# Kernel optimization log

Measured on AMD Instinct MI355X. Metric: run time of the kernel, lower is better.

Reference implementation:

```python
import jax, jax.numpy as jnp
import numpy as np

B, D = 4096, 1024
N_CLASSES = 100
INF = jnp.float32(3.4e38)


def setup_inputs() -> dict:
    key = jax.random.key(0)
    k1, k2 = jax.random.split(key)
    x = jax.random.normal(k1, (B, 1, D), dtype=jnp.float32)
    labels = jax.random.randint(k2, (B,), 0, N_CLASSES)
    return {"x": x, "labels": labels}


def _awareness_scan(xs, labels_f, R_init):
    # xs: [B, D] float32, labels_f: [B] float32
    b, d = xs.shape
    slots = jnp.arange(b)

    def step(state, inp):
        refs, ref_labels, n_refs, count, min_d, max_d, R = state
        xi, li = inp
        mask = slots < n_refs  # active reference slots
        # distances from candidate to current reference set (torch.cdist, p=2)
        d_all = jnp.sqrt(jnp.sum((refs - xi[None, :]) ** 2, axis=-1))  # [B]
        d_all = jax.lax.stop_gradient(d_all)
        d_act = jnp.where(mask, d_all, INF)
        min_act = jnp.min(d_act)
        is_first = count == 1
        # new reference iff ALL active distances exceed R (i.e. min > R)
        insert = is_first | (min_act > R)
        refs2 = jnp.where(insert, refs.at[n_refs].set(xi), refs)
        ref_labels2 = jnp.where(insert, ref_labels.at[n_refs].set(li), ref_labels)
        n_refs2 = n_refs + insert.astype(n_refs.dtype)
        # dynamic ray update (skipped on the very first sample, as in torch)
        max_act = jnp.max(jnp.where(mask, d_all, -INF))
        min_d2 = jnp.where(is_first, min_d, jnp.minimum(min_d, min_act))
        max_d2 = jnp.where(is_first, max_d, jnp.maximum(max_d, max_act))
        R2 = jnp.where(is_first, R, (min_d2 + max_d2) / 3)
        # prediction: nearest reference AFTER potential insertion
        mask2 = slots < n_refs2
        d2 = jnp.sqrt(jnp.sum((refs2 - xi[None, :]) ** 2, axis=-1))
        d2 = jax.lax.stop_gradient(d2)
        idx = jnp.argmin(jnp.where(mask2, d2, INF))
        pred = ref_labels2[idx]
        new_state = (refs2, ref_labels2, n_refs2, count + 1, min_d2, max_d2, R2)
        return new_state, pred

    init = (
        jnp.zeros((b, d), jnp.float32),   # reference instances buffer
        jnp.zeros((b,), jnp.float32),     # reference labels buffer
        jnp.int32(0),                     # n_refs
        jnp.int32(1),                     # count (starts at 1, as in torch)
        INF,                              # min_dist
        jnp.float32(0.0),                 # max_dist
        jnp.float32(R_init),              # R
    )
    _, preds = jax.lax.scan(step, init, (xs, labels_f))
    return preds  # [B] float32


def reference(x, labels):
    # x: [B, 1, D]; labels: [B] int. update_ref_insts=True, set_labels=labels.
    xs = x.reshape(x.shape[0], x.shape[2])
    labels_f = labels.astype(jnp.float32)
    return _awareness_scan(xs, labels_f, 1.0)
```

## Files before the change

kernel.cpp:

```cpp
#include <hip/hip_runtime.h>
#include <stdint.h>

#define B_N   4096
#define D_DIM 1024
#define INF_F 3.4e38f

typedef float floatx4 __attribute__((ext_vector_type(4)));

#define XQ_OFF 131072

__global__ __launch_bounds__(256)
void k_prep(const float* __restrict__ x, unsigned char* __restrict__ xq,
            float* __restrict__ norms,
            unsigned long long* __restrict__ minpack,
            unsigned int* __restrict__ maxbits) {
    const int row = blockIdx.x;
    const int t   = threadIdx.x;
    float4 v = ((const float4*)x)[row * 256 + t];
    int p = __builtin_amdgcn_cvt_pk_fp8_f32(v.x, v.y, 0, false);
    p     = __builtin_amdgcn_cvt_pk_fp8_f32(v.z, v.w, p, true);
    ((int*)xq)[row * 256 + t] = p;
    float s = v.x * v.x + v.y * v.y + v.z * v.z + v.w * v.w;
    #pragma unroll
    for (int off = 32; off; off >>= 1) s += __shfl_down(s, off);
    __shared__ float ws4[4];
    if ((t & 63) == 0) ws4[t >> 6] = s;
    __syncthreads();
    if (t == 0) {
        norms[row]   = ws4[0] + ws4[1] + ws4[2] + ws4[3];
        minpack[row] = 0xFFFFFFFFFFFFFFFFull;
        maxbits[row] = 0u;
    }
}

#define GLDS(g, l)                                                              \
    __builtin_amdgcn_global_load_lds(                                           \
        (__attribute__((address_space(1))) void*)(void*)(g),                    \
        (__attribute__((address_space(3))) void*)(void*)(l), 16, 0, 0)

__global__ __launch_bounds__(256, 2)
void k_pass1_fp8(const unsigned char* __restrict__ xq,
                 const float* __restrict__ norms,
                 unsigned long long* __restrict__ minpack,
                 unsigned int* __restrict__ maxbits) {
    int bid = blockIdx.x;
    int ti  = (int)((sqrtf(8.f * bid + 1.f) - 1.f) * 0.5f);
    while ((ti + 1) * (ti + 2) / 2 <= bid) ti++;
    while (ti * (ti + 1) / 2 > bid) ti--;
    int tj  = bid - ti * (ti + 1) / 2;

    __shared__ unsigned char As[2][16384];
    __shared__ unsigned char Bs[2][16384];
    __shared__ unsigned long long redMin[128][2];
    __shared__ float redMax[128][2];

    const int t    = threadIdx.x;
    const int w    = t >> 6, lane = t & 63;
    const int wm   = w >> 1, wn = w & 1;
    const int q4   = lane >> 4, c15 = lane & 15;
    const int i0   = ti * 128, j0 = tj * 128;

    const int sr = lane >> 3;
    const int sc = (lane & 7) ^ (sr & 7);

    const unsigned char* gA[4]; const unsigned char* gB[4];
    int eoff[4];
    #pragma unroll
    for (int q = 0; q < 4; q++) {
        int e   = w * 4 + q;
        int row = e * 8 + sr;
        gA[q] = xq + (size_t)(i0 + row) * D_DIM + sc * 16;
        gB[q] = xq + (size_t)(j0 + row) * D_DIM + sc * 16;
        eoff[q] = e * 1024;
    }

    const int r7 = c15 & 7;
    int oib[4];
    #pragma unroll
    for (int kk = 0; kk < 4; kk++) {
        int sl  = kk * 2 + (q4 >> 1);
        oib[kk] = (((sl ^ r7) << 4) | ((q4 & 1) << 3));
    }
    int rbA[4], rbB[4];
    #pragma unroll
    for (int st = 0; st < 4; st++) {
        rbA[st] = (wm * 64 + st * 16 + c15) * 128;
        rbB[st] = (wn * 64 + st * 16 + c15) * 128;
    }

    floatx4 acc[4][4];
    #pragma unroll
    for (int m = 0; m < 4; m++)
        #pragma unroll
        for (int n = 0; n < 4; n++)
            acc[m][n] = (floatx4){0.f, 0.f, 0.f, 0.f};

    #pragma unroll
    for (int q = 0; q < 4; q++) {
        GLDS(gA[q], As[0] + eoff[q]);
        GLDS(gB[q], Bs[0] + eoff[q]);
        gA[q] += 128; gB[q] += 128;
    }

    #pragma unroll 2
    for (int it = 0; it < 8; it++) {
        const int p = it & 1;
        if (it < 7) {
            #pragma unroll
            for (int q = 0; q < 4; q++) {
                GLDS(gA[q], As[p ^ 1] + eoff[q]);
                GLDS(gB[q], Bs[p ^ 1] + eoff[q]);
                gA[q] += 128; gB[q] += 128;
            }
            asm volatile("s_waitcnt vmcnt(8)" ::: "memory");
        } else {
            asm volatile("s_waitcnt vmcnt(0)" ::: "memory");
        }
        __builtin_amdgcn_s_barrier();

        const unsigned char* Ap = As[p];
        const unsigned char* Bp = Bs[p];
        #pragma unroll
        for (int kk = 0; kk < 4; kk++) {
            long long af[4], bfr[4];
            #pragma unroll
            for (int st = 0; st < 4; st++) {
                af[st]  = *(const long long*)(Ap + rbA[st] + oib[kk]);
                bfr[st] = *(const long long*)(Bp + rbB[st] + oib[kk]);
            }
            #pragma unroll
            for (int m = 0; m < 4; m++)
                #pragma unroll
                for (int n = 0; n < 4; n++)
                    acc[m][n] = __builtin_amdgcn_mfma_f32_16x16x32_fp8_fp8(
                        af[m], bfr[n], acc[m][n], 0, 0, 0);
        }
        asm volatile("s_waitcnt lgkmcnt(0)" ::: "memory");
        __builtin_amdgcn_s_barrier();
    }

    float nj[4];
    #pragma unroll
    for (int st = 0; st < 4; st++) nj[st] = norms[j0 + wn * 64 + st * 16 + c15];

    #pragma unroll
    for (int st_m = 0; st_m < 4; st_m++) {
        #pragma unroll
        for (int r = 0; r < 4; r++) {
            int i_loc = wm * 64 + st_m * 16 + q4 * 4 + r;
            int gi    = i0 + i_loc;
            float ni  = norms[gi];
            unsigned long long mp = 0xFFFFFFFFFFFFFFFFull;
            float mx = -INF_F;
            #pragma unroll
            for (int st_n = 0; st_n < 4; st_n++) {
                int gj = j0 + wn * 64 + st_n * 16 + c15;
                if (gj < gi) {
                    float dot = acc[st_m][st_n][r];
                    float d2  = fmaxf(ni + nj[st_n] - 2.f * dot, 0.f);
                    unsigned long long p =
                        ((unsigned long long)__float_as_uint(d2) << 32) | (unsigned)gj;
                    if (p < mp) mp = p;
                    mx = fmaxf(mx, d2);
                }
            }
            #pragma unroll
            for (int off = 1; off < 16; off <<= 1) {
                unsigned long long op = __shfl_xor(mp, off, 64);
                if (op < mp) mp = op;
                float om = __shfl_xor(mx, off, 64);
                mx = fmaxf(mx, om);
            }
            if (c15 == 0) { redMin[i_loc][wn] = mp; redMax[i_loc][wn] = mx; }
        }
    }
    __syncthreads();
    if (t < 128) {
        unsigned long long mp = redMin[t][0];
        if (redMin[t][1] < mp) mp = redMin[t][1];
        float mx = fmaxf(redMax[t][0], redMax[t][1]);
        if (mp != 0xFFFFFFFFFFFFFFFFull) {
            atomicMin(&minpack[i0 + t], mp);
            atomicMax(&maxbits[i0 + t], __float_as_uint(mx));
        }
    }
}

__global__ __launch_bounds__(1024)
void k_tail(const unsigned long long* __restrict__ minpack,
            const unsigned int* __restrict__ maxbits,
            const float* __restrict__ x, const float* __restrict__ norms,
            const int* __restrict__ labels, int* __restrict__ ref_idx,
            float* __restrict__ out) {
    const int t    = threadIdx.x;
    const int lane = t & 63, wid = t >> 6;
    float m[4], M[4];
    #pragma unroll
    for (int q = 0; q < 4; q++) {
        int i = t * 4 + q;
        unsigned long long p = minpack[i];
        float dmin = (p == 0xFFFFFFFFFFFFFFFFull)
                       ? INF_F : sqrtf(__uint_as_float((unsigned)(p >> 32)));
        m[q] = (i == 0) ? INF_F : dmin;
        M[q] = (i == 0) ? -INF_F : sqrtf(__uint_as_float(maxbits[i]));
    }
    float pmin[4], pmax[4];
    pmin[0] = m[0]; pmax[0] = M[0];
    #pragma unroll
    for (int q = 1; q < 4; q++) {
        pmin[q] = fminf(pmin[q - 1], m[q]);
        pmax[q] = fmaxf(pmax[q - 1], M[q]);
    }
    float wmin = pmin[3], wmax = pmax[3];
    #pragma unroll
    for (int off = 1; off < 64; off <<= 1) {
        float a = __shfl_up(wmin, off, 64);
        float b = __shfl_up(wmax, off, 64);
        if (lane >= off) { wmin = fminf(wmin, a); wmax = fmaxf(wmax, b); }
    }
    __shared__ float swmin[16], swmax[16];
    if (lane == 63) { swmin[wid] = wmin; swmax[wid] = wmax; }
    __syncthreads();
    float exwMin = INF_F, exwMax = -INF_F;
    for (int k = 0; k < wid; k++) {
        exwMin = fminf(exwMin, swmin[k]);
        exwMax = fmaxf(exwMax, swmax[k]);
    }
    float upMin = __shfl_up(wmin, 1, 64);
    float upMax = __shfl_up(wmax, 1, 64);
    float exMin = fminf(exwMin, (lane > 0) ? upMin : INF_F);
    float exMax = fmaxf(exwMax, (lane > 0) ? upMax : -INF_F);

    int viol = B_N;
    #pragma unroll
    for (int q = 0; q < 4; q++) {
        int i = t * 4 + q;
        if (i >= 1) {
            float pm = (q == 0) ? exMin : fminf(exMin, pmin[q - 1]);
            float pM = (q == 0) ? exMax : fmaxf(exMax, pmax[q - 1]);
            float R  = (i == 1) ? 1.0f : (pm + pM) / 3.0f;
            if (!(m[q] > R) && i < viol) viol = i;
        }
    }
    int vw = viol;
    #pragma unroll
    for (int off = 32; off; off >>= 1) vw = min(vw, __shfl_down(vw, off, 64));
    __shared__ int svw[16];
    if (lane == 0) svw[wid] = vw;
    __syncthreads();
    int s_star = B_N;
    for (int k = 0; k < 16; k++) s_star = min(s_star, svw[k]);

    for (int i = t; i < s_star; i += 1024) out[i] = (float)labels[i];

    __shared__ float s_state[3];
    __shared__ int s_n;
    if (s_star < B_N && t == (s_star >> 2)) {
        int q = s_star & 3;
        float pm = (q == 0) ? exMin : fminf(exMin, pmin[q - 1]);
        float pM = (q == 0) ? exMax : fmaxf(exMax, pmax[q - 1]);
        float md = fminf(pm, m[q]);
        float Md = fmaxf(pM, M[q]);
        s_state[0] = md; s_state[1] = Md; s_state[2] = (md + Md) / 3.0f;
        s_n = s_star;
        unsigned long long p = minpack[s_star];
        int j = (int)(unsigned)(p & 0xFFFFFFFFu);
        out[s_star] = (float)labels[j];
    }
    if (s_star >= B_N) return;

    for (int s = t; s < s_star; s += 1024) ref_idx[s] = s;
    __syncthreads();

    __shared__ unsigned long long redp[1024];
    __shared__ float redm[1024];
    for (int i = s_star + 1; i < B_N; i++) {
        int n = s_n;
        const float* xi = x + (size_t)i * D_DIM;
        float ni = norms[i];
        unsigned long long mp = 0xFFFFFFFFFFFFFFFFull;
        float mx = -INF_F;
        for (int slot = t; slot < n; slot += 1024) {
            int j = ref_idx[slot];
            const float* xj = x + (size_t)j * D_DIM;
            float dot = 0.f;
            for (int k = 0; k < D_DIM; k++) dot = fmaf(xi[k], xj[k], dot);
            float d = sqrtf(fmaxf(ni + norms[j] - 2.f * dot, 0.f));
            unsigned long long p =
                ((unsigned long long)__float_as_uint(d) << 32) | (unsigned)slot;
            if (p < mp) mp = p;
            mx = fmaxf(mx, d);
        }
        redp[t] = mp; redm[t] = mx;
        __syncthreads();
        for (int off = 512; off; off >>= 1) {
            if (t < off) {
                if (redp[t + off] < redp[t]) redp[t] = redp[t + off];
                redm[t] = fmaxf(redm[t], redm[t + off]);
            }
            __syncthreads();
        }
        if (t == 0) {
            unsigned long long p = redp[0];
            float min_act = __uint_as_float((unsigned)(p >> 32));
            int minslot   = (int)(unsigned)(p & 0xFFFFFFFFu);
            float max_act = redm[0];
            bool insert = (min_act > s_state[2]);
            int pred;
            if (insert) {
                ref_idx[n] = i;
                s_n = n + 1;
                pred = (min_act <= 0.0f) ? labels[ref_idx[minslot]] : labels[i];
            } else {
                pred = labels[ref_idx[minslot]];
            }
            float md = fminf(s_state[0], min_act);
            float Md = fmaxf(s_state[1], max_act);
            s_state[0] = md; s_state[1] = Md; s_state[2] = (md + Md) / 3.0f;
            out[i] = (float)pred;
        }
        __syncthreads();
    }
}

extern "C" void kernel_launch(void* const* d_in, const int* in_sizes, int n_in,
                              void* d_out, int out_size, void* d_ws, size_t ws_size,
                              hipStream_t stream) {
    const float* x      = (const float*)d_in[0];
    const int*   labels = (const int*)d_in[1];
    float*       out    = (float*)d_out;
    char* ws = (char*)d_ws;
    unsigned long long* minpack = (unsigned long long*)ws;
    unsigned int*       maxbits = (unsigned int*)(ws + 32768);
    float*              norms   = (float*)(ws + 49152);
    int*                ref_idx = (int*)(ws + 65600);
    unsigned char*      xq      = (unsigned char*)(ws + XQ_OFF);

    k_prep<<<B_N, 256, 0, stream>>>(x, xq, norms, minpack, maxbits);
    const int ntiles  = B_N / 128;
    const int nblocks = ntiles * (ntiles + 1) / 2;
    k_pass1_fp8<<<nblocks, 256, 0, stream>>>(xq, norms, minpack, maxbits);
    k_tail<<<1, 1024, 0, stream>>>(minpack, maxbits, x, norms, labels, ref_idx, out);
}
```

Before: 105.8 us.

## Use 512-thread blocks with single-buffered LDS in fp8 distance pass

The fp8 MFMA Gram kernel now runs 8 waves per block in a 4x2 layout. Each wave computes a 32x64 sub-tile instead of 64x64, which halves the accumulators per thread. The double-buffered LDS prefetch with manual waitcnt is replaced by a single buffer guarded by two __syncthreads per k-step, and launch bounds rise to allow more resident waves. The intent is to hide global-load latency through occupancy rather than software pipelining, at the cost of losing explicit load/compute overlap and adding more barriers.

```diff
diff --git a/kernel.cpp b/kernel.cpp
--- a/kernel.cpp
+++ b/kernel.cpp
@@ -38,7 +38,7 @@
         (__attribute__((address_space(1))) void*)(void*)(g),                    \
         (__attribute__((address_space(3))) void*)(void*)(l), 16, 0, 0)
 
-__global__ __launch_bounds__(256, 2)
+__global__ __launch_bounds__(512, 6)
 void k_pass1_fp8(const unsigned char* __restrict__ xq,
                  const float* __restrict__ norms,
                  unsigned long long* __restrict__ minpack,
@@ -49,8 +49,8 @@
     while (ti * (ti + 1) / 2 > bid) ti--;
     int tj  = bid - ti * (ti + 1) / 2;
 
-    __shared__ unsigned char As[2][16384];
-    __shared__ unsigned char Bs[2][16384];
+    __shared__ unsigned char As[16384];
+    __shared__ unsigned char Bs[16384];
     __shared__ unsigned long long redMin[128][2];
     __shared__ float redMax[128][2];
 
@@ -63,15 +63,16 @@
     const int sr = lane >> 3;
     const int sc = (lane & 7) ^ (sr & 7);
 
-    const unsigned char* gA[4]; const unsigned char* gB[4];
-    int eoff[4];
-    #pragma unroll
-    for (int q = 0; q < 4; q++) {
-        int e   = w * 4 + q;
+    const unsigned char* gA[2]; const unsigned char* gB[2];
+    unsigned char* lA[2]; unsigned char* lB[2];
+    #pragma unroll
+    for (int q = 0; q < 2; q++) {
+        int e   = w * 2 + q;
         int row = e * 8 + sr;
         gA[q] = xq + (size_t)(i0 + row) * D_DIM + sc * 16;
         gB[q] = xq + (size_t)(j0 + row) * D_DIM + sc * 16;
-        eoff[q] = e * 1024;
+        lA[q] = As + e * 1024;
+        lB[q] = Bs + e * 1024;
     }
 
     const int r7 = c15 & 7;
@@ -81,62 +82,44 @@
         int sl  = kk * 2 + (q4 >> 1);
         oib[kk] = (((sl ^ r7) << 4) | ((q4 & 1) << 3));
     }
-    int rbA[4], rbB[4];
-    #pragma unroll
-    for (int st = 0; st < 4; st++) {
-        rbA[st] = (wm * 64 + st * 16 + c15) * 128;
-        rbB[st] = (wn * 64 + st * 16 + c15) * 128;
-    }
-
-    floatx4 acc[4][4];
-    #pragma unroll
-    for (int m = 0; m < 4; m++)
+    int rbA[2], rbB[4];
+    #pragma unroll
+    for (int st = 0; st < 2; st++) rbA[st] = (wm * 32 + st * 16 + c15) * 128;
+    #pragma unroll
+    for (int st = 0; st < 4; st++) rbB[st] = (wn * 64 + st * 16 + c15) * 128;
+
+    floatx4 acc[2][4];
+    #pragma unroll
+    for (int m = 0; m < 2; m++)
         #pragma unroll
         for (int n = 0; n < 4; n++)
             acc[m][n] = (floatx4){0.f, 0.f, 0.f, 0.f};
 
-    #pragma unroll
-    for (int q = 0; q < 4; q++) {
-        GLDS(gA[q], As[0] + eoff[q]);
-        GLDS(gB[q], Bs[0] + eoff[q]);
-        gA[q] += 128; gB[q] += 128;
-    }
-
-    #pragma unroll 2
     for (int it = 0; it < 8; it++) {
-        const int p = it & 1;
-        if (it < 7) {
-            #pragma unroll
-            for (int q = 0; q < 4; q++) {
-                GLDS(gA[q], As[p ^ 1] + eoff[q]);
-                GLDS(gB[q], Bs[p ^ 1] + eoff[q]);
-                gA[q] += 128; gB[q] += 128;
-            }
-            asm volatile("s_waitcnt vmcnt(8)" ::: "memory");
-        } else {
-            asm volatile("s_waitcnt vmcnt(0)" ::: "memory");
-        }
-        __builtin_amdgcn_s_barrier();
-
-        const unsigned char* Ap = As[p];
-        const unsigned char* Bp = Bs[p];
+        __syncthreads();
+        #pragma unroll
+        for (int q = 0; q < 2; q++) {
+            GLDS(gA[q], lA[q]);
+            GLDS(gB[q], lB[q]);
+            gA[q] += 128; gB[q] += 128;
+        }
+        __syncthreads();
         #pragma unroll
         for (int kk = 0; kk < 4; kk++) {
-            long long af[4], bfr[4];
-            #pragma unroll
-            for (int st = 0; st < 4; st++) {
-                af[st]  = *(const long long*)(Ap + rbA[st] + oib[kk]);
-                bfr[st] = *(const long long*)(Bp + rbB[st] + oib[kk]);
-            }
-            #pragma unroll
-            for (int m = 0; m < 4; m++)
+            long long af[2], bfr[4];
+            #pragma unroll
+            for (int st = 0; st < 2; st++)
+                af[st]  = *(const long long*)(As + rbA[st] + oib[kk]);
+            #pragma unroll
+            for (int st = 0; st < 4; st++)
+                bfr[st] = *(const long long*)(Bs + rbB[st] + oib[kk]);
+            #pragma unroll
+            for (int m = 0; m < 2; m++)
                 #pragma unroll
                 for (int n = 0; n < 4; n++)
                     acc[m][n] = __builtin_amdgcn_mfma_f32_16x16x32_fp8_fp8(
                         af[m], bfr[n], acc[m][n], 0, 0, 0);
         }
-        asm volatile("s_waitcnt lgkmcnt(0)" ::: "memory");
-        __builtin_amdgcn_s_barrier();
     }
 
     float nj[4];
@@ -144,10 +127,10 @@
     for (int st = 0; st < 4; st++) nj[st] = norms[j0 + wn * 64 + st * 16 + c15];
 
     #pragma unroll
-    for (int st_m = 0; st_m < 4; st_m++) {
+    for (int st_m = 0; st_m < 2; st_m++) {
         #pragma unroll
         for (int r = 0; r < 4; r++) {
-            int i_loc = wm * 64 + st_m * 16 + q4 * 4 + r;
+            int i_loc = wm * 32 + st_m * 16 + q4 * 4 + r;
             int gi    = i0 + i_loc;
             float ni  = norms[gi];
             unsigned long long mp = 0xFFFFFFFFFFFFFFFFull;
@@ -339,6 +322,6 @@
     k_prep<<<B_N, 256, 0, stream>>>(x, xq, norms, minpack, maxbits);
     const int ntiles  = B_N / 128;
     const int nblocks = ntiles * (ntiles + 1) / 2;
-    k_pass1_fp8<<<nblocks, 256, 0, stream>>>(xq, norms, minpack, maxbits);
+    k_pass1_fp8<<<nblocks, 512, 0, stream>>>(xq, norms, minpack, maxbits);
     k_tail<<<1, 1024, 0, stream>>>(minpack, maxbits, x, norms, labels, ref_idx, out);
 }
```

Measured after the change: 98.45 us. 7.0% less time.
